# Performance work log

Hardware: AMD Instinct MI355X
Metric: run time of the kernel (lower is better)

## Reference

```python
import jax, jax.numpy as jnp
import numpy as np
from jax import lax

EMBED_DIM = 1024
NUM_HEADS = 8
KEY_DIM = EMBED_DIM // NUM_HEADS  # 128
B, H, W = 2, 48, 48
N = H * W


def _rope(t, sin, cos):
    # t: [..., d]; sin/cos broadcastable to t
    x1 = t[..., ::2]
    x2 = t[..., 1::2]
    rot = jnp.stack([-x2, x1], axis=-1).reshape(t.shape)  # interleave (-x2, x1)
    return t * cos - rot * sin


def setup_inputs() -> dict:
    key = jax.random.key(0)
    ks = jax.random.split(key, 16)
    C = EMBED_DIM
    w = 0.02
    return {
        "x": jax.random.normal(ks[0], (B, H, W, C), jnp.float32),
        "sin": jax.random.normal(ks[1], (H, W, KEY_DIM), jnp.float32),
        "cos": jax.random.normal(ks[2], (H, W, KEY_DIM), jnp.float32),
        "mask": jax.random.normal(ks[3], (NUM_HEADS, N, N), jnp.float32),
        "Wq": jax.random.normal(ks[4], (C, C), jnp.float32) * w,
        "bq": jax.random.normal(ks[5], (C,), jnp.float32) * w,
        "Wk": jax.random.normal(ks[6], (C, C), jnp.float32) * w,
        "bk": jax.random.normal(ks[7], (C,), jnp.float32) * w,
        "Wv": jax.random.normal(ks[8], (C, C), jnp.float32) * w,
        "bv": jax.random.normal(ks[9], (C,), jnp.float32) * w,
        "lepe_w": jax.random.normal(ks[10], (5, 5, 1, C), jnp.float32) * w,  # HWIO, groups=C
        "lepe_b": jax.random.normal(ks[11], (C,), jnp.float32) * w,
        "Wo": jax.random.normal(ks[12], (C, C), jnp.float32) * w,
        "bo": jnp.zeros((C,), jnp.float32),
    }


def reference(x, sin, cos, mask, Wq, bq, Wk, bk, Wv, bv, lepe_w, lepe_b, Wo, bo):
    Bb, Hh, Ww, C = x.shape
    nh, kd = NUM_HEADS, KEY_DIM
    scaling = kd ** -0.5

    q = x @ Wq.T + bq                     # [B,H,W,C]
    k = (x @ Wk.T + bk) * scaling         # [B,H,W,C]
    v = x @ Wv.T + bv                     # [B,H,W,C]

    # depthwise 5x5 lepe on NHWC
    lepe = lax.conv_general_dilated(
        v, lepe_w, window_strides=(1, 1), padding="SAME",
        dimension_numbers=("NHWC", "HWIO", "NHWC"),
        feature_group_count=C,
    ) + lepe_b

    # [B,H,W,C] -> [B,nh,H,W,kd]
    qh = q.reshape(Bb, Hh, Ww, nh, kd).transpose(0, 3, 1, 2, 4)
    kh = k.reshape(Bb, Hh, Ww, nh, kd).transpose(0, 3, 1, 2, 4)

    sin_ = sin[None, None]  # [1,1,H,W,kd]
    cos_ = cos[None, None]
    qh = _rope(qh, sin_, cos_)
    kh = _rope(kh, sin_, cos_)

    qf = qh.reshape(Bb, nh, Hh * Ww, kd)  # [B,nh,N,kd]
    kf = kh.reshape(Bb, nh, Hh * Ww, kd)
    vf = v.reshape(Bb, Hh, Ww, nh, kd).transpose(0, 3, 1, 2, 4).reshape(Bb, nh, Hh * Ww, kd)

    attn = jnp.einsum("bhnd,bhmd->bhnm", qf, kf) + mask  # [B,nh,N,N]
    attn = jax.nn.softmax(attn, axis=-1)
    out = jnp.einsum("bhnm,bhmd->bhnd", attn, vf)         # [B,nh,N,kd]

    out = out.transpose(0, 2, 1, 3).reshape(Bb, Hh, Ww, nh * kd)
    out = out + lepe
    return out @ Wo.T + bo
```

## Files before the change

kernel.cpp:

```cpp
#include <hip/hip_runtime.h>
#include <hip/hip_bf16.h>
#include <stdint.h>

typedef __bf16 bf16_t;
typedef __bf16 bf16x8 __attribute__((ext_vector_type(8)));
typedef __bf16 bf16x4 __attribute__((ext_vector_type(4)));
typedef float f32x4 __attribute__((ext_vector_type(4)));
typedef unsigned int u32x4 __attribute__((ext_vector_type(4)));

#define MFMA16(A, B, C) __builtin_amdgcn_mfma_f32_16x16x32_bf16(A, B, C, 0, 0, 0)

__device__ inline void dma16(const void* g, void* l) {
    __builtin_amdgcn_global_load_lds(
        (const __attribute__((address_space(1))) unsigned int*)g,
        (__attribute__((address_space(3))) unsigned int*)l, 16, 0, 0);
}

__device__ inline unsigned pack2(float a, float b) {
    unsigned short ua = __builtin_bit_cast(unsigned short, (bf16_t)a);
    unsigned short ub = __builtin_bit_cast(unsigned short, (bf16_t)b);
    return (unsigned)ua | ((unsigned)ub << 16);
}

__global__ __launch_bounds__(256)
void cvt_kernel(const float* __restrict__ in, bf16_t* __restrict__ outp, int n8)
{
    int i = blockIdx.x * 256 + threadIdx.x;
    if (i >= n8) return;
    const float* p = in + (size_t)i * 8;
    f32x4 a = *(const f32x4*)p;
    f32x4 b = *(const f32x4*)(p + 4);
    bf16x8 r;
    r[0] = (bf16_t)a[0]; r[1] = (bf16_t)a[1]; r[2] = (bf16_t)a[2]; r[3] = (bf16_t)a[3];
    r[4] = (bf16_t)b[0]; r[5] = (bf16_t)b[1]; r[6] = (bf16_t)b[2]; r[7] = (bf16_t)b[3];
    *(bf16x8*)(outp + (size_t)i * 8) = r;
}

__global__ __launch_bounds__(256)
void cvt4_kernel(const float* __restrict__ W0, const float* __restrict__ W1,
                 const float* __restrict__ W2, const float* __restrict__ W3,
                 bf16_t* __restrict__ outp)
{
    int i = blockIdx.x * 256 + threadIdx.x;
    int sel = i >> 17;
    int j = i & 131071;
    const float* src = sel == 0 ? W0 : sel == 1 ? W1 : sel == 2 ? W2 : W3;
    const float* p = src + (size_t)j * 8;
    f32x4 a = *(const f32x4*)p;
    f32x4 b = *(const f32x4*)(p + 4);
    bf16x8 r;
    r[0] = (bf16_t)a[0]; r[1] = (bf16_t)a[1]; r[2] = (bf16_t)a[2]; r[3] = (bf16_t)a[3];
    r[4] = (bf16_t)b[0]; r[5] = (bf16_t)b[1]; r[6] = (bf16_t)b[2]; r[7] = (bf16_t)b[3];
    *(bf16x8*)(outp + (size_t)i * 8) = r;
}

__device__ __forceinline__
void gemm_core64(const bf16_t* __restrict__ A, const bf16_t* __restrict__ W,
                 const float* __restrict__ bias, void* __restrict__ outp,
                 int mode, float scale,
                 const float* __restrict__ sinp, const float* __restrict__ cosp,
                 int m0, int n0, char* lds)
{
    const int K = 1024;
    const int ASZ = 4096, BUF = 12288;
    const int t = threadIdx.x;
    const int w = t >> 6, l = t & 63;
    const int wm = w >> 1, wn = w & 1;
    const int lr = l & 15;
    const int kch = (l >> 4) * 8;

    const f32x4 zz = {0.f, 0.f, 0.f, 0.f};
    f32x4 acc[2][4];
#pragma unroll
    for (int i = 0; i < 2; i++)
#pragma unroll
        for (int j = 0; j < 4; j++) acc[i][j] = zz;

    dma16(A + (size_t)(m0 + w * 16 + lr) * K + kch, lds + w * 1024);
#pragma unroll
    for (int i = 0; i < 2; i++) {
        int f = w * 2 + i;
        dma16(W + (size_t)(n0 + f * 16 + lr) * K + kch, lds + ASZ + f * 1024);
    }
    __syncthreads();

    int bo = 0;
    for (int k0 = 0; k0 < K; k0 += 32) {
        int kn = k0 + 32;
        if (kn < K) {
            int nb = bo ^ BUF;
            dma16(A + (size_t)(m0 + w * 16 + lr) * K + kn + kch, lds + nb + w * 1024);
#pragma unroll
            for (int i = 0; i < 2; i++) {
                int f = w * 2 + i;
                dma16(W + (size_t)(n0 + f * 16 + lr) * K + kn + kch, lds + nb + ASZ + f * 1024);
            }
        }
        bf16x8 af[2], bfg[4];
#pragma unroll
        for (int mt = 0; mt < 2; mt++)
            af[mt] = *(const bf16x8*)(lds + bo + ((wm * 2 + mt) * 64 + l) * 16);
#pragma unroll
        for (int nt = 0; nt < 4; nt++)
            bfg[nt] = *(const bf16x8*)(lds + bo + ASZ + ((wn * 4 + nt) * 64 + l) * 16);
#pragma unroll
        for (int mt = 0; mt < 2; mt++)
#pragma unroll
            for (int nt = 0; nt < 4; nt++)
                acc[mt][nt] = MFMA16(af[mt], bfg[nt], acc[mt][nt]);
        __syncthreads();
        bo ^= BUF;
    }

    const int quad = l >> 4, lc = l & 15;
#pragma unroll
    for (int mt = 0; mt < 2; mt++) {
#pragma unroll
        for (int nt = 0; nt < 4; nt++) {
            int gn = n0 + wn * 64 + nt * 16 + lc;
            float bv = bias[gn];
            int gm0 = m0 + wm * 32 + mt * 16 + quad * 4;
            if (mode == 0) {
                float* o32 = (float*)outp;
#pragma unroll
                for (int r = 0; r < 4; r++)
                    o32[(size_t)(gm0 + r) * 1024 + gn] = acc[mt][nt][r] + bv;
            } else if (mode == 1) {
                bf16_t* ob = (bf16_t*)outp;
                int h = gn >> 7, d = gn & 127;
#pragma unroll
                for (int r = 0; r < 4; r++) {
                    int gm = gm0 + r;
                    int b = gm / 2304;
                    int pos = gm - b * 2304;
                    float val = acc[mt][nt][r] + bv;
                    float pv = __shfl_xor(val, 1);
                    float sn = sinp[pos * 128 + d];
                    float cs = cosp[pos * 128 + d];
                    float res = (d & 1) ? (val * cs - pv * sn) : (val * cs + pv * sn);
                    ob[(((size_t)b * 8 + h) * 2304 + pos) * 128 + d] = (bf16_t)(res * scale);
                }
            } else {
                bf16_t* ob = (bf16_t*)outp;
                int h = gn >> 7, d = gn & 127;
                int b = gm0 / 2304;
                int pos0 = gm0 - b * 2304;
                bf16x4 s4;
#pragma unroll
                for (int r = 0; r < 4; r++)
                    s4[r] = (bf16_t)(acc[mt][nt][r] + bv);
                *(bf16x4*)(ob + (((size_t)b * 8 + h) * 128 + d) * 2304 + pos0) = s4;
            }
        }
    }
}

__global__ __launch_bounds__(256)
void gemm_bt_kernel(const bf16_t* __restrict__ A, const bf16_t* __restrict__ W,
                    const float* __restrict__ bias, void* __restrict__ outp,
                    int mode, float scale,
                    const float* __restrict__ sinp, const float* __restrict__ cosp)
{
    __shared__ __align__(16) char lds[24576];
    gemm_core64(A, W, bias, outp, mode, scale, sinp, cosp,
                blockIdx.x * 64, blockIdx.y * 128, lds);
}

__global__ __launch_bounds__(256)
void gemm_qkv_kernel(const bf16_t* __restrict__ A, const bf16_t* __restrict__ Wall,
                     const float* __restrict__ bq, const float* __restrict__ bk,
                     const float* __restrict__ bv,
                     void* __restrict__ qb, void* __restrict__ kb, void* __restrict__ vtb,
                     const float* __restrict__ sinp, const float* __restrict__ cosp,
                     float kscale)
{
    __shared__ __align__(16) char lds[24576];
    int ny = blockIdx.y;
    int third = ny >> 3;
    int n0 = (ny & 7) * 128;
    const bf16_t* W = Wall + (size_t)third * 1048576;
    const float* bias = third == 0 ? bq : third == 1 ? bk : bv;
    void* outp = third == 0 ? qb : third == 1 ? kb : vtb;
    int mode = third == 2 ? 2 : 1;
    float scale = third == 1 ? kscale : 1.0f;
    gemm_core64(A, W, bias, outp, mode, scale, sinp, cosp, blockIdx.x * 64, n0, lds);
}

__global__ __launch_bounds__(512, 4)
void attn_kernel(const bf16_t* __restrict__ q, const bf16_t* __restrict__ k,
                 const bf16_t* __restrict__ vt, const float* __restrict__ mask,
                 bf16_t* __restrict__ o)
{
    const int N = 2304;
    const int HK = 1152;
    __shared__ __align__(16) char lds[65536];

    const int t = threadIdx.x;
    const int w = t >> 6, l = t & 63;
    const int hv = w >> 2, wl = w & 3;
    const int quad = l >> 4, lc = l & 15;

    int gid = blockIdx.x;
    int grp = gid >> 4, sub = gid & 15;
    int u = grp * 8 + (sub & 7);
    int b = sub >> 3;
    int qblk = u >> 3, h = u & 7;
    int bh = b * 8 + h;
    int q0 = qblk * 64;

    const int qrow = q0 + wl * 16 + lc;

    const bf16_t* qb = q + (size_t)bh * N * 128;
    const bf16_t* kb = k + (size_t)bh * N * 128 + (size_t)hv * HK * 128;
    const bf16_t* vtb = vt + (size_t)bh * 128 * N + hv * HK;
    const float* mq = mask + (size_t)h * N * N + (size_t)qrow * N + hv * HK + quad * 4;

    char* Ks = lds + hv * 32768;
    char* Vts = Ks + 16384;

    bf16x8 qf[4];
#pragma unroll
    for (int kc = 0; kc < 4; kc++)
        qf[kc] = *(const bf16x8*)(qb + (size_t)qrow * 128 + kc * 32 + quad * 8);

    f32x4 mv[4], mvn[4];
#pragma unroll
    for (int nt = 0; nt < 4; nt++)
        mv[nt] = *(const f32x4*)(mq + nt * 16);

    const f32x4 zz = {0.f, 0.f, 0.f, 0.f};
    float Mr = -1e30f, Lr = 0.f;
    f32x4 Oacc[8];
#pragma unroll
    for (int i = 0; i < 8; i++) Oacc[i] = zz;

    for (int kv0 = 0; kv0 < HK; kv0 += 64) {
        __syncthreads();
#pragma unroll
        for (int i = 0; i < 4; i++) {
            int f = wl * 4 + i;
            dma16(kb + (size_t)(kv0 + (f >> 2) * 16 + lc) * 128 + (f & 3) * 32 + quad * 8,
                  Ks + f * 1024);
            dma16(vtb + (size_t)((f >> 1) * 16 + lc) * N + kv0 + (f & 1) * 32 + quad * 8,
                  Vts + f * 1024);
        }
        __syncthreads();
        int nxt = kv0 + 64;
        if (nxt < HK) {
#pragma unroll
            for (int nt = 0; nt < 4; nt++)
                mvn[nt] = *(const f32x4*)(mq + nxt + nt * 16);
        }

        f32x4 s[4];
#pragma unroll
        for (int nt = 0; nt < 4; nt++) {
            f32x4 a = zz;
#pragma unroll
            for (int kc = 0; kc < 4; kc++) {
                bf16x8 kf = *(const bf16x8*)(Ks + ((nt * 4 + kc) * 64 + l) * 16);
                a = MFMA16(kf, qf[kc], a);
            }
            s[nt] = a + mv[nt];
        }

        float mx = fmaxf(fmaxf(fmaxf(s[0][0], s[0][1]), fmaxf(s[0][2], s[0][3])),
                         fmaxf(fmaxf(s[1][0], s[1][1]), fmaxf(s[1][2], s[1][3])));
        mx = fmaxf(mx, fmaxf(fmaxf(fmaxf(s[2][0], s[2][1]), fmaxf(s[2][2], s[2][3])),
                             fmaxf(fmaxf(s[3][0], s[3][1]), fmaxf(s[3][2], s[3][3]))));
        mx = fmaxf(mx, __shfl_xor(mx, 16));
        mx = fmaxf(mx, __shfl_xor(mx, 32));
        float mnew = fmaxf(Mr, mx);
        float alpha = __expf(Mr - mnew);
        Mr = mnew;

        float rs = 0.f;
        unsigned pw[4][2];
#pragma unroll
        for (int nt = 0; nt < 4; nt++) {
            float p0 = __expf(s[nt][0] - mnew);
            float p1 = __expf(s[nt][1] - mnew);
            float p2 = __expf(s[nt][2] - mnew);
            float p3 = __expf(s[nt][3] - mnew);
            rs += (p0 + p1) + (p2 + p3);
            pw[nt][0] = pack2(p0, p1);
            pw[nt][1] = pack2(p2, p3);
        }
        rs += __shfl_xor(rs, 16);
        rs += __shfl_xor(rs, 32);
        Lr = Lr * alpha + rs;

#pragma unroll
        for (int dt = 0; dt < 8; dt++)
#pragma unroll
            for (int r = 0; r < 4; r++)
                Oacc[dt][r] *= alpha;

#pragma unroll
        for (int pc = 0; pc < 2; pc++) {
            u32x4 wv;
#pragma unroll
            for (int jp = 0; jp < 4; jp++) {
                int src = ((quad & 1) * 2 + (jp >> 1)) * 16 + lc;
                int t0 = __shfl((int)pw[pc * 2 + 0][jp & 1], src);
                int t1 = __shfl((int)pw[pc * 2 + 1][jp & 1], src);
                wv[jp] = (quad >> 1) ? (unsigned)t1 : (unsigned)t0;
            }
            bf16x8 pf = __builtin_bit_cast(bf16x8, wv);
#pragma unroll
            for (int dt = 0; dt < 8; dt++) {
                bf16x8 vf = *(const bf16x8*)(Vts + ((dt * 2 + pc) * 64 + l) * 16);
                Oacc[dt] = MFMA16(vf, pf, Oacc[dt]);
            }
        }

        if (nxt < HK) {
#pragma unroll
            for (int nt = 0; nt < 4; nt++) mv[nt] = mvn[nt];
        }
    }

    __syncthreads();
    float* Ml = (float*)(lds + 32768);
    if (hv == 1) {
        float* ob = (float*)(lds + wl * 8192);
#pragma unroll
        for (int dt = 0; dt < 8; dt++)
            *(f32x4*)(ob + (size_t)(dt * 64 + l) * 4) = Oacc[dt];
        if (quad == 0) {
            Ml[wl * 16 + lc] = Mr;
            Ml[64 + wl * 16 + lc] = Lr;
        }
    }
    __syncthreads();
    if (hv == 0) {
        const float* ob = (const float*)(lds + wl * 8192);
        float M1 = Ml[wl * 16 + lc];
        float L1 = Ml[64 + wl * 16 + lc];
        float M = fmaxf(Mr, M1);
        float w0 = __expf(Mr - M), w1 = __expf(M1 - M);
        float inv = 1.f / (Lr * w0 + L1 * w1);
#pragma unroll
        for (int dt = 0; dt < 8; dt++) {
            f32x4 o1 = *(const f32x4*)(ob + (size_t)(dt * 64 + l) * 4);
            bf16x4 s4;
#pragma unroll
            for (int r = 0; r < 4; r++)
                s4[r] = (bf16_t)((Oacc[dt][r] * w0 + o1[r] * w1) * inv);
            *(bf16x4*)(o + ((size_t)b * N + qrow) * 1024 + h * 128 + dt * 16 + quad * 4) = s4;
        }
    }
}

__global__ __launch_bounds__(256)
void lepe_kernel(const bf16_t* __restrict__ vt, const float* __restrict__ wgt,
                 const float* __restrict__ lb, const bf16_t* __restrict__ o,
                 bf16_t* __restrict__ ab)
{
    __shared__ __align__(16) bf16_t sv[5 * 48 * 128];
    const int bh = blockIdx.y;
    const int b = bh >> 3, h = bh & 7;
    const int y0 = blockIdx.x;
    const int t = threadIdx.x;

#pragma unroll
    for (int it = 0; it < 15; it++) {
        int idx = t + it * 256;
        int ck = idx % 6;
        int dy = idx / 6;
        int d = dy & 127, yloc = dy >> 7;
        int y = y0 - 2 + yloc;
        bf16x8 vvv;
#pragma unroll
        for (int j = 0; j < 8; j++) vvv[j] = (bf16_t)0.f;
        if (y >= 0 && y < 48)
            vvv = *(const bf16x8*)(vt + ((size_t)bh * 128 + d) * 2304 + y * 48 + ck * 8);
        int x0 = ck * 8;
#pragma unroll
        for (int j = 0; j < 8; j++)
            sv[(yloc * 48 + x0 + j) * 128 + d] = vvv[j];
    }
    __syncthreads();

    const int d0 = (t & 15) * 8;
    const int xb = t >> 4;
    float acc[3][8];
    f32x4 b0 = *(const f32x4*)(lb + h * 128 + d0);
    f32x4 b1 = *(const f32x4*)(lb + h * 128 + d0 + 4);
#pragma unroll
    for (int c = 0; c < 3; c++)
#pragma unroll
        for (int j = 0; j < 4; j++) { acc[c][j] = b0[j]; acc[c][4 + j] = b1[j]; }

#pragma unroll
    for (int ky = 0; ky < 5; ky++) {
#pragma unroll
        for (int kx = 0; kx < 5; kx++) {
            const float* wp = wgt + (size_t)(ky * 5 + kx) * 1024 + h * 128 + d0;
            f32x4 w0 = *(const f32x4*)wp;
            f32x4 w1 = *(const f32x4*)(wp + 4);
#pragma unroll
            for (int c = 0; c < 3; c++) {
                int xx = xb + c * 16 + kx - 2;
                if (xx < 0 || xx >= 48) continue;
                bf16x8 vv = *(const bf16x8*)(&sv[(ky * 48 + xx) * 128 + d0]);
#pragma unroll
                for (int j = 0; j < 4; j++) {
                    acc[c][j]     += (float)vv[j]     * w0[j];
                    acc[c][4 + j] += (float)vv[4 + j] * w1[j];
                }
            }
        }
    }
#pragma unroll
    for (int c = 0; c < 3; c++) {
        int x = xb + c * 16;
        size_t off = ((size_t)b * 2304 + y0 * 48 + x) * 1024 + h * 128 + d0;
        bf16x8 ov = *(const bf16x8*)(o + off);
        bf16x8 res;
#pragma unroll
        for (int j = 0; j < 8; j++) res[j] = (bf16_t)(acc[c][j] + (float)ov[j]);
        *(bf16x8*)(ab + off) = res;
    }
}

extern "C" void kernel_launch(void* const* d_in, const int* in_sizes, int n_in,
                              void* d_out, int out_size, void* d_ws, size_t ws_size,
                              hipStream_t stream)
{
    const float* x    = (const float*)d_in[0];
    const float* sin_ = (const float*)d_in[1];
    const float* cos_ = (const float*)d_in[2];
    const float* mask = (const float*)d_in[3];
    const float* Wq   = (const float*)d_in[4];
    const float* bq   = (const float*)d_in[5];
    const float* Wk   = (const float*)d_in[6];
    const float* bk   = (const float*)d_in[7];
    const float* Wv   = (const float*)d_in[8];
    const float* bv   = (const float*)d_in[9];
    const float* lw   = (const float*)d_in[10];
    const float* lb   = (const float*)d_in[11];
    const float* Wo   = (const float*)d_in[12];
    const float* bo   = (const float*)d_in[13];

    const size_t NB = (size_t)2 * 2304 * 1024;

    bf16_t* dout_b = (bf16_t*)d_out;
    bf16_t* x16 = dout_b;
    bf16_t* vtb = dout_b + NB;
    bf16_t* ob  = dout_b;

    bf16_t* qb   = (bf16_t*)d_ws;
    bf16_t* kb   = qb + NB;
    bf16_t* wbuf = kb + NB;
    bf16_t* ab   = qb;

    dim3 blk(256);
    const float kscale = 0.08838834764831845f;

    cvt_kernel<<<2304, blk, 0, stream>>>(x, x16, 589824);
    cvt4_kernel<<<2048, blk, 0, stream>>>(Wq, Wk, Wv, Wo, wbuf);
    gemm_qkv_kernel<<<dim3(72, 24), blk, 0, stream>>>(x16, wbuf, bq, bk, bv,
                                                      qb, kb, vtb, sin_, cos_, kscale);
    attn_kernel<<<576, dim3(512), 0, stream>>>(qb, kb, vtb, mask, ob);
    lepe_kernel<<<dim3(48, 16), blk, 0, stream>>>(vtb, lw, lb, ob, ab);
    gemm_bt_kernel<<<dim3(72, 8), blk, 0, stream>>>(ab, wbuf + 3 * 1048576, bo,
                                                    d_out, 0, 1.0f, nullptr, nullptr);
}
```

Baseline: 571.9 us.

## Deepen GEMM K-stage to 64 and give attention waves two query fragments

```diff
diff --git a/kernel.cpp b/kernel.cpp
--- a/kernel.cpp
+++ b/kernel.cpp
@@ -62,7 +62,7 @@
                  int m0, int n0, char* lds)
 {
     const int K = 1024;
-    const int ASZ = 4096, BUF = 12288;
+    const int ASZ = 8192, BUF = 24576;
     const int t = threadIdx.x;
     const int w = t >> 6, l = t & 63;
     const int wm = w >> 1, wn = w & 1;
@@ -76,41 +76,51 @@
 #pragma unroll
         for (int j = 0; j < 4; j++) acc[i][j] = zz;
 
-    dma16(A + (size_t)(m0 + w * 16 + lr) * K + kch, lds + w * 1024);
-#pragma unroll
-    for (int i = 0; i < 2; i++) {
-        int f = w * 2 + i;
-        dma16(W + (size_t)(n0 + f * 16 + lr) * K + kch, lds + ASZ + f * 1024);
-    }
+#define GSTAGE(base, kk)                                                        \
+    {                                                                           \
+        int a0 = w * 2;                                                         \
+        dma16(A + (size_t)(m0 + (a0 >> 1) * 16 + lr) * K + (kk) + (a0 & 1) * 32 + kch, \
+              (base) + a0 * 1024);                                              \
+        int a1 = w * 2 + 1;                                                     \
+        dma16(A + (size_t)(m0 + (a1 >> 1) * 16 + lr) * K + (kk) + (a1 & 1) * 32 + kch, \
+              (base) + a1 * 1024);                                              \
+        _Pragma("unroll")                                                       \
+        for (int i = 0; i < 4; i++) {                                           \
+            int f = w * 4 + i;                                                  \
+            dma16(W + (size_t)(n0 + (f >> 1) * 16 + lr) * K + (kk) + (f & 1) * 32 + kch, \
+                  (base) + ASZ + f * 1024);                                     \
+        }                                                                       \
+    }
+
+    GSTAGE(lds, 0);
     __syncthreads();
 
     int bo = 0;
-    for (int k0 = 0; k0 < K; k0 += 32) {
-        int kn = k0 + 32;
+    for (int k0 = 0; k0 < K; k0 += 64) {
+        int kn = k0 + 64;
         if (kn < K) {
-            int nb = bo ^ BUF;
-            dma16(A + (size_t)(m0 + w * 16 + lr) * K + kn + kch, lds + nb + w * 1024);
-#pragma unroll
-            for (int i = 0; i < 2; i++) {
-                int f = w * 2 + i;
-                dma16(W + (size_t)(n0 + f * 16 + lr) * K + kn + kch, lds + nb + ASZ + f * 1024);
-            }
-        }
-        bf16x8 af[2], bfg[4];
-#pragma unroll
-        for (int mt = 0; mt < 2; mt++)
-            af[mt] = *(const bf16x8*)(lds + bo + ((wm * 2 + mt) * 64 + l) * 16);
-#pragma unroll
-        for (int nt = 0; nt < 4; nt++)
-            bfg[nt] = *(const bf16x8*)(lds + bo + ASZ + ((wn * 4 + nt) * 64 + l) * 16);
-#pragma unroll
-        for (int mt = 0; mt < 2; mt++)
+            char* nb = lds + (bo ^ BUF);
+            GSTAGE(nb, kn);
+        }
+#pragma unroll
+        for (int kh = 0; kh < 2; kh++) {
+            bf16x8 af[2], bfg[4];
+#pragma unroll
+            for (int mt = 0; mt < 2; mt++)
+                af[mt] = *(const bf16x8*)(lds + bo + (((wm * 2 + mt) * 2 + kh) * 64 + l) * 16);
 #pragma unroll
             for (int nt = 0; nt < 4; nt++)
-                acc[mt][nt] = MFMA16(af[mt], bfg[nt], acc[mt][nt]);
+                bfg[nt] = *(const bf16x8*)(lds + bo + ASZ + (((wn * 4 + nt) * 2 + kh) * 64 + l) * 16);
+#pragma unroll
+            for (int mt = 0; mt < 2; mt++)
+#pragma unroll
+                for (int nt = 0; nt < 4; nt++)
+                    acc[mt][nt] = MFMA16(af[mt], bfg[nt], acc[mt][nt]);
+        }
         __syncthreads();
         bo ^= BUF;
     }
+#undef GSTAGE
 
     const int quad = l >> 4, lc = l & 15;
 #pragma unroll
@@ -161,7 +171,7 @@
                     int mode, float scale,
                     const float* __restrict__ sinp, const float* __restrict__ cosp)
 {
-    __shared__ __align__(16) char lds[24576];
+    __shared__ __align__(16) char lds[49152];
     gemm_core64(A, W, bias, outp, mode, scale, sinp, cosp,
                 blockIdx.x * 64, blockIdx.y * 128, lds);
 }
@@ -174,7 +184,7 @@
                      const float* __restrict__ sinp, const float* __restrict__ cosp,
                      float kscale)
 {
-    __shared__ __align__(16) char lds[24576];
+    __shared__ __align__(16) char lds[49152];
     int ny = blockIdx.y;
     int third = ny >> 3;
     int n0 = (ny & 7) * 128;
@@ -186,7 +196,7 @@
     gemm_core64(A, W, bias, outp, mode, scale, sinp, cosp, blockIdx.x * 64, n0, lds);
 }
 
-__global__ __launch_bounds__(512, 4)
+__global__ __launch_bounds__(256, 2)
 void attn_kernel(const bf16_t* __restrict__ q, const bf16_t* __restrict__ k,
                  const bf16_t* __restrict__ vt, const float* __restrict__ mask,
                  bf16_t* __restrict__ o)
@@ -197,7 +207,7 @@
 
     const int t = threadIdx.x;
     const int w = t >> 6, l = t & 63;
-    const int hv = w >> 2, wl = w & 3;
+    const int hv = w >> 1, wl = w & 1;
     const int quad = l >> 4, lc = l & 15;
 
     int gid = blockIdx.x;
@@ -208,146 +218,183 @@
     int bh = b * 8 + h;
     int q0 = qblk * 64;
 
-    const int qrow = q0 + wl * 16 + lc;
+    int qrow0 = q0 + wl * 32 + lc;
+    int qrow1 = qrow0 + 16;
 
     const bf16_t* qb = q + (size_t)bh * N * 128;
     const bf16_t* kb = k + (size_t)bh * N * 128 + (size_t)hv * HK * 128;
     const bf16_t* vtb = vt + (size_t)bh * 128 * N + hv * HK;
-    const float* mq = mask + (size_t)h * N * N + (size_t)qrow * N + hv * HK + quad * 4;
+    const float* mq0 = mask + (size_t)h * N * N + (size_t)qrow0 * N + hv * HK + quad * 4;
+    const float* mq1 = mq0 + (size_t)16 * N;
 
     char* Ks = lds + hv * 32768;
     char* Vts = Ks + 16384;
 
-    bf16x8 qf[4];
-#pragma unroll
-    for (int kc = 0; kc < 4; kc++)
-        qf[kc] = *(const bf16x8*)(qb + (size_t)qrow * 128 + kc * 32 + quad * 8);
-
-    f32x4 mv[4], mvn[4];
-#pragma unroll
-    for (int nt = 0; nt < 4; nt++)
-        mv[nt] = *(const f32x4*)(mq + nt * 16);
+    bf16x8 qf[2][4];
+#pragma unroll
+    for (int kc = 0; kc < 4; kc++) {
+        qf[0][kc] = *(const bf16x8*)(qb + (size_t)qrow0 * 128 + kc * 32 + quad * 8);
+        qf[1][kc] = *(const bf16x8*)(qb + (size_t)qrow1 * 128 + kc * 32 + quad * 8);
+    }
 
     const f32x4 zz = {0.f, 0.f, 0.f, 0.f};
-    float Mr = -1e30f, Lr = 0.f;
-    f32x4 Oacc[8];
-#pragma unroll
-    for (int i = 0; i < 8; i++) Oacc[i] = zz;
+    float Mr0 = -1e30f, Mr1 = -1e30f, Lr0 = 0.f, Lr1 = 0.f;
+    f32x4 Oacc[2][8];
+#pragma unroll
+    for (int fr = 0; fr < 2; fr++)
+#pragma unroll
+        for (int i = 0; i < 8; i++) Oacc[fr][i] = zz;
 
     for (int kv0 = 0; kv0 < HK; kv0 += 64) {
         __syncthreads();
 #pragma unroll
-        for (int i = 0; i < 4; i++) {
-            int f = wl * 4 + i;
+        for (int i = 0; i < 8; i++) {
+            int f = wl * 8 + i;
             dma16(kb + (size_t)(kv0 + (f >> 2) * 16 + lc) * 128 + (f & 3) * 32 + quad * 8,
                   Ks + f * 1024);
             dma16(vtb + (size_t)((f >> 1) * 16 + lc) * N + kv0 + (f & 1) * 32 + quad * 8,
                   Vts + f * 1024);
         }
         __syncthreads();
-        int nxt = kv0 + 64;
-        if (nxt < HK) {
-#pragma unroll
-            for (int nt = 0; nt < 4; nt++)
-                mvn[nt] = *(const f32x4*)(mq + nxt + nt * 16);
-        }
-
-        f32x4 s[4];
+
+        f32x4 mv0[4], mv1[4];
 #pragma unroll
         for (int nt = 0; nt < 4; nt++) {
-            f32x4 a = zz;
+            mv0[nt] = *(const f32x4*)(mq0 + kv0 + nt * 16);
+            mv1[nt] = *(const f32x4*)(mq1 + kv0 + nt * 16);
+        }
+
+        f32x4 s0[4], s1[4];
+#pragma unroll
+        for (int nt = 0; nt < 4; nt++) {
+            f32x4 a0 = zz, a1 = zz;
 #pragma unroll
             for (int kc = 0; kc < 4; kc++) {
                 bf16x8 kf = *(const bf16x8*)(Ks + ((nt * 4 + kc) * 64 + l) * 16);
-                a = MFMA16(kf, qf[kc], a);
+                a0 = MFMA16(kf, qf[0][kc], a0);
+                a1 = MFMA16(kf, qf[1][kc], a1);
             }
-            s[nt] = a + mv[nt];
-        }
-
-        float mx = fmaxf(fmaxf(fmaxf(s[0][0], s[0][1]), fmaxf(s[0][2], s[0][3])),
-                         fmaxf(fmaxf(s[1][0], s[1][1]), fmaxf(s[1][2], s[1][3])));
-        mx = fmaxf(mx, fmaxf(fmaxf(fmaxf(s[2][0], s[2][1]), fmaxf(s[2][2], s[2][3])),
-                             fmaxf(fmaxf(s[3][0], s[3][1]), fmaxf(s[3][2], s[3][3]))));
-        mx = fmaxf(mx, __shfl_xor(mx, 16));
-        mx = fmaxf(mx, __shfl_xor(mx, 32));
-        float mnew = fmaxf(Mr, mx);
-        float alpha = __expf(Mr - mnew);
-        Mr = mnew;
-
-        float rs = 0.f;
-        unsigned pw[4][2];
+            s0[nt] = a0 + mv0[nt];
+            s1[nt] = a1 + mv1[nt];
+        }
+
+        float mx0 = fmaxf(fmaxf(fmaxf(s0[0][0], s0[0][1]), fmaxf(s0[0][2], s0[0][3])),
+                          fmaxf(fmaxf(s0[1][0], s0[1][1]), fmaxf(s0[1][2], s0[1][3])));
+        mx0 = fmaxf(mx0, fmaxf(fmaxf(fmaxf(s0[2][0], s0[2][1]), fmaxf(s0[2][2], s0[2][3])),
+                               fmaxf(fmaxf(s0[3][0], s0[3][1]), fmaxf(s0[3][2], s0[3][3]))));
+        float mx1 = fmaxf(fmaxf(fmaxf(s1[0][0], s1[0][1]), fmaxf(s1[0][2], s1[0][3])),
+                          fmaxf(fmaxf(s1[1][0], s1[1][1]), fmaxf(s1[1][2], s1[1][3])));
+        mx1 = fmaxf(mx1, fmaxf(fmaxf(fmaxf(s1[2][0], s1[2][1]), fmaxf(s1[2][2], s1[2][3])),
+                               fmaxf(fmaxf(s1[3][0], s1[3][1]), fmaxf(s1[3][2], s1[3][3]))));
+        mx0 = fmaxf(mx0, __shfl_xor(mx0, 16));
+        mx1 = fmaxf(mx1, __shfl_xor(mx1, 16));
+        mx0 = fmaxf(mx0, __shfl_xor(mx0, 32));
+        mx1 = fmaxf(mx1, __shfl_xor(mx1, 32));
+
+        int small = (mx0 <= Mr0 + 8.f) && (mx1 <= Mr1 + 8.f);
+        float al0 = 1.f, al1 = 1.f;
+        if (!__all(small)) {
+            float mn0 = fmaxf(Mr0, mx0), mn1 = fmaxf(Mr1, mx1);
+            al0 = __expf(Mr0 - mn0);
+            al1 = __expf(Mr1 - mn1);
+            Mr0 = mn0; Mr1 = mn1;
+#pragma unroll
+            for (int dt = 0; dt < 8; dt++)
+#pragma unroll
+                for (int r = 0; r < 4; r++) {
+                    Oacc[0][dt][r] *= al0;
+                    Oacc[1][dt][r] *= al1;
+                }
+        }
+
+        float rs0 = 0.f, rs1 = 0.f;
+        unsigned pw0[4][2], pw1[4][2];
 #pragma unroll
         for (int nt = 0; nt < 4; nt++) {
-            float p0 = __expf(s[nt][0] - mnew);
-            float p1 = __expf(s[nt][1] - mnew);
-            float p2 = __expf(s[nt][2] - mnew);
-            float p3 = __expf(s[nt][3] - mnew);
-            rs += (p0 + p1) + (p2 + p3);
-            pw[nt][0] = pack2(p0, p1);
-            pw[nt][1] = pack2(p2, p3);
-        }
-        rs += __shfl_xor(rs, 16);
-        rs += __shfl_xor(rs, 32);
-        Lr = Lr * alpha + rs;
-
-#pragma unroll
-        for (int dt = 0; dt < 8; dt++)
-#pragma unroll
-            for (int r = 0; r < 4; r++)
-                Oacc[dt][r] *= alpha;
+            float p0 = __expf(s0[nt][0] - Mr0);
+            float p1 = __expf(s0[nt][1] - Mr0);
+            float p2 = __expf(s0[nt][2] - Mr0);
+            float p3 = __expf(s0[nt][3] - Mr0);
+            float t0 = __expf(s1[nt][0] - Mr1);
+            float t1 = __expf(s1[nt][1] - Mr1);
+            float t2 = __expf(s1[nt][2] - Mr1);
+            float t3 = __expf(s1[nt][3] - Mr1);
+            rs0 += (p0 + p1) + (p2 + p3);
+            rs1 += (t0 + t1) + (t2 + t3);
+            pw0[nt][0] = pack2(p0, p1);
+            pw0[nt][1] = pack2(p2, p3);
+            pw1[nt][0] = pack2(t0, t1);
+            pw1[nt][1] = pack2(t2, t3);
+        }
+        rs0 += __shfl_xor(rs0, 16);
+        rs1 += __shfl_xor(rs1, 16);
+        rs0 += __shfl_xor(rs0, 32);
+        rs1 += __shfl_xor(rs1, 32);
+        Lr0 = Lr0 * al0 + rs0;
+        Lr1 = Lr1 * al1 + rs1;
 
 #pragma unroll
         for (int pc = 0; pc < 2; pc++) {
-            u32x4 wv;
+            u32x4 wv0, wv1;
 #pragma unroll
             for (int jp = 0; jp < 4; jp++) {
                 int src = ((quad & 1) * 2 + (jp >> 1)) * 16 + lc;
-                int t0 = __shfl((int)pw[pc * 2 + 0][jp & 1], src);
-                int t1 = __shfl((int)pw[pc * 2 + 1][jp & 1], src);
-                wv[jp] = (quad >> 1) ? (unsigned)t1 : (unsigned)t0;
+                int a0 = __shfl((int)pw0[pc * 2 + 0][jp & 1], src);
+                int a1 = __shfl((int)pw0[pc * 2 + 1][jp & 1], src);
+                int c0 = __shfl((int)pw1[pc * 2 + 0][jp & 1], src);
+                int c1 = __shfl((int)pw1[pc * 2 + 1][jp & 1], src);
+                wv0[jp] = (quad >> 1) ? (unsigned)a1 : (unsigned)a0;
+                wv1[jp] = (quad >> 1) ? (unsigned)c1 : (unsigned)c0;
             }
-            bf16x8 pf = __builtin_bit_cast(bf16x8, wv);
+            bf16x8 pf0 = __builtin_bit_cast(bf16x8, wv0);
+            bf16x8 pf1 = __builtin_bit_cast(bf16x8, wv1);
 #pragma unroll
             for (int dt = 0; dt < 8; dt++) {
                 bf16x8 vf = *(const bf16x8*)(Vts + ((dt * 2 + pc) * 64 + l) * 16);
-                Oacc[dt] = MFMA16(vf, pf, Oacc[dt]);
+                Oacc[0][dt] = MFMA16(vf, pf0, Oacc[0][dt]);
+                Oacc[1][dt] = MFMA16(vf, pf1, Oacc[1][dt]);
             }
-        }
-
-        if (nxt < HK) {
-#pragma unroll
-            for (int nt = 0; nt < 4; nt++) mv[nt] = mvn[nt];
         }
     }
 
     __syncthreads();
     float* Ml = (float*)(lds + 32768);
     if (hv == 1) {
-        float* ob = (float*)(lds + wl * 8192);
-#pragma unroll
-        for (int dt = 0; dt < 8; dt++)
-            *(f32x4*)(ob + (size_t)(dt * 64 + l) * 4) = Oacc[dt];
+        float* ob = (float*)lds;
+#pragma unroll
+        for (int fr = 0; fr < 2; fr++)
+#pragma unroll
+            for (int dt = 0; dt < 8; dt++)
+                *(f32x4*)(ob + (size_t)(((wl * 2 + fr) * 8 + dt) * 64 + l) * 4) = Oacc[fr][dt];
         if (quad == 0) {
-            Ml[wl * 16 + lc] = Mr;
-            Ml[64 + wl * 16 + lc] = Lr;
+            Ml[wl * 32 + lc]       = Mr0;
+            Ml[wl * 32 + 16 + lc]  = Mr1;
+            Ml[128 + wl * 32 + lc]      = Lr0;
+            Ml[128 + wl * 32 + 16 + lc] = Lr1;
         }
     }
     __syncthreads();
     if (hv == 0) {
-        const float* ob = (const float*)(lds + wl * 8192);
-        float M1 = Ml[wl * 16 + lc];
-        float L1 = Ml[64 + wl * 16 + lc];
-        float M = fmaxf(Mr, M1);
-        float w0 = __expf(Mr - M), w1 = __expf(M1 - M);
-        float inv = 1.f / (Lr * w0 + L1 * w1);
-#pragma unroll
-        for (int dt = 0; dt < 8; dt++) {
-            f32x4 o1 = *(const f32x4*)(ob + (size_t)(dt * 64 + l) * 4);
-            bf16x4 s4;
-#pragma unroll
-            for (int r = 0; r < 4; r++)
-                s4[r] = (bf16_t)((Oacc[dt][r] * w0 + o1[r] * w1) * inv);
-            *(bf16x4*)(o + ((size_t)b * N + qrow) * 1024 + h * 128 + dt * 16 + quad * 4) = s4;
+        const float* ob = (const float*)lds;
+#pragma unroll
+        for (int fr = 0; fr < 2; fr++) {
+            float Mh = fr ? Mr1 : Mr0;
+            float Lh = fr ? Lr1 : Lr0;
+            int qrow = fr ? qrow1 : qrow0;
+            float M1 = Ml[wl * 32 + fr * 16 + lc];
+            float L1 = Ml[128 + wl * 32 + fr * 16 + lc];
+            float M = fmaxf(Mh, M1);
+            float w0 = __expf(Mh - M), w1 = __expf(M1 - M);
+            float inv = 1.f / (Lh * w0 + L1 * w1);
+#pragma unroll
+            for (int dt = 0; dt < 8; dt++) {
+                f32x4 o1 = *(const f32x4*)(ob + (size_t)(((wl * 2 + fr) * 8 + dt) * 64 + l) * 4);
+                bf16x4 s4;
+#pragma unroll
+                for (int r = 0; r < 4; r++)
+                    s4[r] = (bf16_t)((Oacc[fr][dt][r] * w0 + o1[r] * w1) * inv);
+                *(bf16x4*)(o + ((size_t)b * N + qrow) * 1024 + h * 128 + dt * 16 + quad * 4) = s4;
+            }
         }
     }
 }
@@ -462,7 +509,7 @@
     cvt4_kernel<<<2048, blk, 0, stream>>>(Wq, Wk, Wv, Wo, wbuf);
     gemm_qkv_kernel<<<dim3(72, 24), blk, 0, stream>>>(x16, wbuf, bq, bk, bv,
                                                       qb, kb, vtb, sin_, cos_, kscale);
-    attn_kernel<<<576, dim3(512), 0, stream>>>(qb, kb, vtb, mask, ob);
+    attn_kernel<<<576, blk, 0, stream>>>(qb, kb, vtb, mask, ob);
     lepe_kernel<<<dim3(48, 16), blk, 0, stream>>>(vtb, lw, lb, ob, ab);
     gemm_bt_kernel<<<dim3(72, 8), blk, 0, stream>>>(ab, wbuf + 3 * 1048576, bo,
                                                     d_out, 0, 1.0f, nullptr, nullptr);
```

Result: slower. 596.4 us (+4.3%).
